# Kernel tuning notes

Hardware: AMD Instinct MI355X
Metric: run time of the kernel (lower is better)

Reference implementation:

```python
import jax, jax.numpy as jnp
import numpy as np

B, S, L, H, D, DF = 2, 1024, 2, 8, 512, 2048
DK = D // H  # head dim (dk == dv == 64)
EPS = 1e-5


def _ln(x, g, b):
    m = jnp.mean(x, axis=-1, keepdims=True)
    v = jnp.mean((x - m) ** 2, axis=-1, keepdims=True)
    return (x - m) / jnp.sqrt(v + EPS) * g + b


def setup_inputs() -> dict:
    key = jax.random.key(0)
    ks = jax.random.split(key, 8)
    sd = 1.0 / np.sqrt(D)
    sf = 1.0 / np.sqrt(DF)
    inp = {
        "src": jax.random.normal(ks[0], (B, S, D), jnp.float32),
        "Wq": jax.random.normal(ks[1], (L, D, D), jnp.float32) * sd,
        "bq": jnp.zeros((L, D), jnp.float32),
        "Wk": jax.random.normal(ks[2], (L, D, D), jnp.float32) * sd,
        "bk": jnp.zeros((L, D), jnp.float32),
        "Wv": jax.random.normal(ks[3], (L, D, D), jnp.float32) * sd,
        "bv": jnp.zeros((L, D), jnp.float32),
        "Wo": jax.random.normal(ks[4], (L, D, D), jnp.float32) * sd,
        "bo": jnp.zeros((L, D), jnp.float32),
        "W1": jax.random.normal(ks[5], (L, D, DF), jnp.float32) * sd,
        "b1": jnp.zeros((L, DF), jnp.float32),
        "W2": jax.random.normal(ks[6], (L, DF, D), jnp.float32) * sf,
        "b2": jnp.zeros((L, D), jnp.float32),
        "g1": jnp.ones((L, D), jnp.float32),
        "be1": jnp.zeros((L, D), jnp.float32),
        "g2": jnp.ones((L, D), jnp.float32),
        "be2": jnp.zeros((L, D), jnp.float32),
        "gf": jnp.ones((D,), jnp.float32),
        "bef": jnp.zeros((D,), jnp.float32),
    }
    return inp


def _heads(x):
    # [B,S,D] -> [B,H,S,DK]
    return x.reshape(B, S, H, DK).transpose(0, 2, 1, 3)


def _causal_linear_attention(q, k, v):
    # Faithful to torch: cumsum of per-step KV outer products, then query contraction.
    kv = jnp.einsum("bhsk,bhsv->bhskv", k, v)      # [B,H,S,DK,DK]
    cum = jnp.cumsum(kv, axis=2)                     # prefix sums over sequence
    return jnp.einsum("bhsk,bhskv->bhsv", q, cum)   # [B,H,S,DK]


def reference(src, Wq, bq, Wk, bk, Wv, bv, Wo, bo, W1, b1, W2, b2,
              g1, be1, g2, be2, gf, bef):
    x = src
    for i in range(L):
        q = _heads(x @ Wq[i] + bq[i])
        k = _heads(x @ Wk[i] + bk[i])
        v = _heads(x @ Wv[i] + bv[i])
        att = _causal_linear_attention(q, k, v)
        att = att.transpose(0, 2, 1, 3).reshape(B, S, D)
        att = att @ Wo[i] + bo[i]
        x = _ln(x + att, g1[i], be1[i])              # post-norm (normalize_before=False)
        ff = jax.nn.relu(x @ W1[i] + b1[i]) @ W2[i] + b2[i]
        x = _ln(x + ff, g2[i], be2[i])
    return _ln(x, gf, bef)                            # final encoder LayerNorm
```

## Files before the change

kernel.cpp:

```cpp
#include <hip/hip_runtime.h>
#include <hip/hip_bf16.h>

#define DEV static __device__ __forceinline__

typedef __attribute__((ext_vector_type(8))) short short8;
typedef __attribute__((ext_vector_type(4))) float f32x4;

DEV unsigned short f2b(float f){
  unsigned int u = __float_as_uint(f);
  return (unsigned short)((u + 0x7FFFu + ((u >> 16) & 1u)) >> 16);
}
DEV float b2f(unsigned short h){ return __uint_as_float(((unsigned int)h) << 16); }
DEV float load_in(const void* p, size_t i, int isbf){
  return isbf ? b2f(((const unsigned short*)p)[i]) : ((const float*)p)[i];
}
DEV void load_lds16(const unsigned short* g, unsigned short* l){
  __builtin_amdgcn_global_load_lds(
      (const __attribute__((address_space(1))) void*)g,
      (__attribute__((address_space(3))) void*)l, 16, 0, 0);
}

DEV int detect_isbf_block(const void* src){
  __shared__ int cnt[4];
  int tid = threadIdx.x;
  float v = b2f(((const unsigned short*)src)[2 * tid]);
  float av = fabsf(v);
  bool sane = ((av < 64.0f) && (av > 9.5e-7f)) || (v == 0.0f);
  unsigned long long m = __ballot(sane);
  if ((tid & 63) == 0) cnt[tid >> 6] = __popcll(m);
  __syncthreads();
  int tot = cnt[0] + cnt[1] + cnt[2] + cnt[3];
  __syncthreads();
  return tot > 128;
}

struct WDesc { const void* src; long src_off; unsigned short* dst; int K; int N; int tstart; };
struct SDesc { const void* src; int src_off; int dstart; };
struct IngestParams {
  WDesc w[12];
  SDesc s[22];
  float* sdst; int stotal;
  const void* src;
  float* xf; unsigned short* xb;
};

__global__ __launch_bounds__(256) void ingest_all(IngestParams P){
  __shared__ float tile[32][33];
  int b = blockIdx.x, tid = threadIdx.x;
  int isbf = detect_isbf_block(P.src);
  if (b < 6144){
    int t = 0;
    #pragma unroll
    for (int i = 1; i < 12; ++i) if (b >= P.w[i].tstart) t = i;
    WDesc d = P.w[t];
    int r = b - d.tstart;
    int tiles_x = d.N >> 5;
    int tx = r % tiles_x, ty = r / tiles_x;
    int lx = tid & 31, ly = tid >> 5;
    #pragma unroll
    for (int i = 0; i < 4; ++i){
      int row = ty*32 + ly + i*8;
      int col = tx*32 + lx;
      tile[ly + i*8][lx] = load_in(d.src, (size_t)d.src_off + (size_t)row*d.N + col, isbf);
    }
    __syncthreads();
    #pragma unroll
    for (int i = 0; i < 4; ++i){
      int orow = tx*32 + ly + i*8;
      int ocol = ty*32 + lx;
      d.dst[(size_t)orow*d.K + ocol] = f2b(tile[lx][ly + i*8]);
    }
    return;
  }
  int mb = b - 6144;
  if (mb < 4096){
    int i = mb*256 + tid;
    float v = load_in(P.src, (size_t)i, isbf);
    P.xf[i] = v; P.xb[i] = f2b(v);
  } else {
    int i = (mb - 4096)*256 + tid;
    if (i < P.stotal){
      int t = 0;
      #pragma unroll
      for (int j = 1; j < 22; ++j) if (i >= P.s[j].dstart) t = j;
      P.sdst[i] = load_in(P.s[t].src, (size_t)P.s[t].src_off + (i - P.s[t].dstart), isbf);
    }
  }
}

struct GemmArgs {
  const unsigned short* A;
  const unsigned short* Bt;
  const float* bias;
  float* Cf;
  unsigned short* Cb;
  int K;
  int lda, ldb, ldc;
  int cshift, cmask;
  size_t cstride;
  size_t cfz;
  int relu;
};

template<int BN>
__global__ __launch_bounds__(256) void gemm_bt(GemmArgs g){
  constexpr int NI = (BN == 128) ? 4 : 2;
  constexpr int NJ = 4;
  constexpr int BPASS = BN / 32;
  __shared__ __align__(16) unsigned short sA[2][128*64];
  __shared__ __align__(16) unsigned short sB[2][BN*64];
  int tid = threadIdx.x;
  int koff = blockIdx.z * g.K;
  int K = g.K, lda = g.lda, ldb = g.ldb;
  size_t bm = (size_t)blockIdx.y * 128, bn = (size_t)blockIdx.x * BN;
  int lane = tid & 63, wv = tid >> 6, quad = lane >> 4, l16 = lane & 15;
  int wm = (BN == 128) ? (wv >> 1) * 64 : wv * 32;
  int wn = (BN == 128) ? (wv & 1) * 64 : 0;
  f32x4 acc[NI][NJ];
  #pragma unroll
  for (int i=0;i<NI;++i)
    #pragma unroll
    for (int j=0;j<NJ;++j) acc[i][j] = (f32x4){0.f,0.f,0.f,0.f};
  int srow = tid >> 3;
  int schunk = (tid & 7) ^ (srow & 7);
  const unsigned short* Ap = g.A  + (bm + srow)*lda + koff + schunk*8;
  const unsigned short* Bp = g.Bt + (bn + srow)*ldb + koff + schunk*8;

  #define STAGE(buf, ko)                                                      \
    do {                                                                      \
      _Pragma("unroll")                                                       \
      for (int p = 0; p < 4; ++p)                                             \
        load_lds16(Ap + (size_t)(p*32)*lda + (ko), &sA[buf][p*2048 + tid*8]); \
      _Pragma("unroll")                                                       \
      for (int p = 0; p < BPASS; ++p)                                         \
        load_lds16(Bp + (size_t)(p*32)*ldb + (ko), &sB[buf][p*2048 + tid*8]); \
    } while (0)

  STAGE(0, 0);
  asm volatile("s_waitcnt vmcnt(0)" ::: "memory");
  __builtin_amdgcn_s_barrier();

  int nt = K >> 6;
  int cur = 0;
  for (int t = 0; t < nt; ++t){
    if (t + 1 < nt){
      STAGE(cur ^ 1, (t + 1) * 64);
      __builtin_amdgcn_sched_barrier(0);
    }
    #pragma unroll
    for (int kk = 0; kk < 2; ++kk){
      short8 af[NI], bfv[NJ];
      #pragma unroll
      for (int i=0;i<NI;++i){
        int row = wm + i*16 + l16;
        int ch  = (kk*4 + quad) ^ (row & 7);
        af[i] = *(const short8*)&sA[cur][row*64 + ch*8];
      }
      #pragma unroll
      for (int j=0;j<NJ;++j){
        int row = wn + j*16 + l16;
        int ch  = (kk*4 + quad) ^ (row & 7);
        bfv[j] = *(const short8*)&sB[cur][row*64 + ch*8];
      }
      #pragma unroll
      for (int i=0;i<NI;++i)
        #pragma unroll
        for (int j=0;j<NJ;++j)
          acc[i][j] = __builtin_amdgcn_mfma_f32_16x16x32_bf16(af[i], bfv[j], acc[i][j], 0,0,0);
    }
    if (t + 1 < nt){
      asm volatile("s_waitcnt vmcnt(0)" ::: "memory");
      __builtin_amdgcn_s_barrier();
    }
    cur ^= 1;
  }
  #undef STAGE

  float* Cf = g.Cf ? g.Cf + (size_t)blockIdx.z * g.cfz : nullptr;
  unsigned short* Cb = g.Cb;
  #pragma unroll
  for (int j=0;j<NJ;++j){
    int col = (int)bn + wn + j*16 + l16;
    float bv = g.bias ? g.bias[col] : 0.f;
    size_t cbase = ((size_t)(col >> g.cshift))*g.cstride + (col & g.cmask);
    #pragma unroll
    for (int i=0;i<NI;++i){
      #pragma unroll
      for (int r=0;r<4;++r){
        int row = (int)bm + wm + i*16 + quad*4 + r;
        float v = acc[i][j][r] + bv;
        if (g.relu) v = fmaxf(v, 0.f);
        size_t idx = cbase + (size_t)row*g.ldc;
        if (Cf) Cf[idx] = v;
        if (Cb) Cb[idx] = f2b(v);
      }
    }
  }
}

#define ATT_S 1024
#define ATT_D 512

__global__ __launch_bounds__(256) void attn_state_kernel(
    const unsigned short* k, const unsigned short* v, float* states)
{
  __shared__ __align__(16) unsigned short sVt[64*72];
  __shared__ __align__(16) unsigned short sKt[64*72];
  int tid = threadIdx.x;
  int c = blockIdx.x, bh = blockIdx.y;
  int b = bh >> 3, h = bh & 7;
  const size_t base = ((size_t)b*ATT_S + (size_t)c*64)*ATT_D + h*64;
  int lane = tid & 63, wv = tid >> 6, quad = lane >> 4, l16 = lane & 15;

  int t = lane, vc = wv*8;
  const unsigned short* vp = v + base + (size_t)t*ATT_D;
  const unsigned short* kp = k + base + (size_t)t*ATT_D;
  float4 v0 = *(const float4*)(vp + vc);
  float4 v1 = *(const float4*)(vp + vc + 32);
  float4 k0 = *(const float4*)(kp + vc);
  float4 k1 = *(const float4*)(kp + vc + 32);
  {
    const unsigned short* pv0 = (const unsigned short*)&v0;
    const unsigned short* pv1 = (const unsigned short*)&v1;
    const unsigned short* pk0 = (const unsigned short*)&k0;
    const unsigned short* pk1 = (const unsigned short*)&k1;
    #pragma unroll
    for (int e = 0; e < 8; ++e){
      sVt[(vc+e)*72 + t]    = pv0[e];
      sVt[(vc+32+e)*72 + t] = pv1[e];
      sKt[(vc+e)*72 + t]    = pk0[e];
      sKt[(vc+32+e)*72 + t] = pk1[e];
    }
  }
  __syncthreads();

  f32x4 acc[4];
  #pragma unroll
  for (int j=0;j<4;++j) acc[j] = (f32x4){0.f,0.f,0.f,0.f};
  #pragma unroll
  for (int kk=0;kk<2;++kk){
    short8 a = *(const short8*)&sVt[(wv*16 + l16)*72 + kk*32 + quad*8];
    #pragma unroll
    for (int j=0;j<4;++j){
      short8 bb = *(const short8*)&sKt[(j*16 + l16)*72 + kk*32 + quad*8];
      acc[j] = __builtin_amdgcn_mfma_f32_16x16x32_bf16(a, bb, acc[j], 0,0,0);
    }
  }
  float* st = states + ((size_t)bh*16 + c)*4096;
  #pragma unroll
  for (int j=0;j<4;++j)
    #pragma unroll
    for (int rr=0;rr<4;++rr)
      st[(wv*16 + quad*4 + rr)*64 + j*16 + l16] = acc[j][rr];
}

__global__ __launch_bounds__(256) void attn_out_kernel(
    const unsigned short* q, const unsigned short* k, const unsigned short* v,
    const float* states, unsigned short* att)
{
  __shared__ __align__(16) unsigned short sQ [64*72];
  __shared__ __align__(16) unsigned short sK [64*72];
  __shared__ __align__(16) unsigned short sVt[64*72];
  __shared__ __align__(16) float sKV[64*68];
  int tid = threadIdx.x;
  int c = blockIdx.x, bh = blockIdx.y;
  int b = bh >> 3, h = bh & 7;
  const size_t base = ((size_t)b*ATT_S + (size_t)c*64)*ATT_D + h*64;
  int lane = tid & 63, wv = tid >> 6, quad = lane >> 4, l16 = lane & 15;

  float4 racc[4];
  #pragma unroll
  for (int u=0;u<4;++u) racc[u] = (float4){0.f,0.f,0.f,0.f};
  const float* sbase = states + (size_t)bh*16*4096;
  for (int cc = 0; cc < c; ++cc){
    const float4* sp = (const float4*)(sbase + (size_t)cc*4096);
    #pragma unroll
    for (int u=0;u<4;++u){
      float4 t4 = sp[tid + u*256];
      racc[u].x += t4.x; racc[u].y += t4.y; racc[u].z += t4.z; racc[u].w += t4.w;
    }
  }
  #pragma unroll
  for (int u=0;u<4;++u){
    int e = (tid + u*256)*4;
    int row = e >> 6, col = e & 63;
    *(float4*)&sKV[row*68 + col] = racc[u];
  }

  int r = tid >> 2, c8 = (tid & 3)*8;
  const unsigned short* qp = q + base + (size_t)r*ATT_D;
  const unsigned short* kp = k + base + (size_t)r*ATT_D;
  float4 q0 = *(const float4*)(qp + c8);
  float4 q1 = *(const float4*)(qp + c8 + 32);
  float4 k0 = *(const float4*)(kp + c8);
  float4 k1 = *(const float4*)(kp + c8 + 32);
  int t = lane, vc = wv*8;
  const unsigned short* vp = v + base + (size_t)t*ATT_D;
  float4 v0 = *(const float4*)(vp + vc);
  float4 v1 = *(const float4*)(vp + vc + 32);
  *(float4*)&sQ[r*72 + c8]      = q0;
  *(float4*)&sQ[r*72 + c8 + 32] = q1;
  *(float4*)&sK[r*72 + c8]      = k0;
  *(float4*)&sK[r*72 + c8 + 32] = k1;
  {
    const unsigned short* pv0 = (const unsigned short*)&v0;
    const unsigned short* pv1 = (const unsigned short*)&v1;
    #pragma unroll
    for (int e=0;e<8;++e){
      sVt[(vc+e)*72 + t]    = pv0[e];
      sVt[(vc+32+e)*72 + t] = pv1[e];
    }
  }
  __syncthreads();

  f32x4 accS[4];
  #pragma unroll
  for (int j=0;j<4;++j) accS[j] = (f32x4){0.f,0.f,0.f,0.f};
  #pragma unroll
  for (int kk=0;kk<2;++kk){
    short8 a = *(const short8*)&sQ[(wv*16 + l16)*72 + kk*32 + quad*8];
    #pragma unroll
    for (int j=0;j<4;++j){
      short8 bb = *(const short8*)&sK[(j*16 + l16)*72 + kk*32 + quad*8];
      accS[j] = __builtin_amdgcn_mfma_f32_16x16x32_bf16(a, bb, accS[j], 0,0,0);
    }
  }
  __syncthreads();

  #pragma unroll
  for (int j=0;j<4;++j)
    #pragma unroll
    for (int rr=0;rr<4;++rr){
      int i  = wv*16 + quad*4 + rr;
      int cj = j*16 + l16;
      sK[i*72 + cj] = f2b((i >= cj) ? accS[j][rr] : 0.f);
    }

  f32x4 accO[4];
  #pragma unroll
  for (int j=0;j<4;++j) accO[j] = (f32x4){0.f,0.f,0.f,0.f};
  #pragma unroll
  for (int kk=0;kk<2;++kk){
    short8 a = *(const short8*)&sQ[(wv*16 + l16)*72 + kk*32 + quad*8];
    #pragma unroll
    for (int j=0;j<4;++j){
      const float* pf = &sKV[(j*16 + l16)*68 + kk*32 + quad*8];
      short8 bb;
      #pragma unroll
      for (int e=0;e<8;++e) ((unsigned short*)&bb)[e] = f2b(pf[e]);
      accO[j] = __builtin_amdgcn_mfma_f32_16x16x32_bf16(a, bb, accO[j], 0,0,0);
    }
  }
  __syncthreads();

  #pragma unroll
  for (int kk=0;kk<2;++kk){
    short8 a = *(const short8*)&sK[(wv*16 + l16)*72 + kk*32 + quad*8];
    #pragma unroll
    for (int j=0;j<4;++j){
      short8 bb = *(const short8*)&sVt[(j*16 + l16)*72 + kk*32 + quad*8];
      accO[j] = __builtin_amdgcn_mfma_f32_16x16x32_bf16(a, bb, accO[j], 0,0,0);
    }
  }
  #pragma unroll
  for (int j=0;j<4;++j)
    #pragma unroll
    for (int rr=0;rr<4;++rr){
      int i  = wv*16 + quad*4 + rr;
      int cj = j*16 + l16;
      att[base + (size_t)i*ATT_D + cj] = f2b(accO[j][rr]);
    }
}

__global__ __launch_bounds__(256) void add_ln_kernel(
    const float* x, const float* p, int np, const float* bias,
    const float* g, const float* bta, const float* g2, const float* b2,
    float* outf, unsigned short* outb, void* outd, const void* dsrc, int rows)
{
  int isbf = 0;
  if (dsrc) isbf = detect_isbf_block(dsrc);
  int row = blockIdx.x*4 + (threadIdx.x >> 6);
  int lane = threadIdx.x & 63;
  if (row >= rows) return;
  const float* xr = x + (size_t)row*512;
  float a[8];
  *(float4*)&a[0] = *(const float4*)(xr + lane*4);
  *(float4*)&a[4] = *(const float4*)(xr + 256 + lane*4);
  for (int s = 0; s < np; ++s){
    const float* pr = p + (size_t)s*1048576 + (size_t)row*512;
    float yb[8];
    *(float4*)&yb[0] = *(const float4*)(pr + lane*4);
    *(float4*)&yb[4] = *(const float4*)(pr + 256 + lane*4);
    #pragma unroll
    for (int e=0;e<8;++e) a[e] += yb[e];
  }
  if (bias){
    float bb2[8];
    *(float4*)&bb2[0] = *(const float4*)(bias + lane*4);
    *(float4*)&bb2[4] = *(const float4*)(bias + 256 + lane*4);
    #pragma unroll
    for (int e=0;e<8;++e) a[e] += bb2[e];
  }
  float s = 0.f, qq = 0.f;
  #pragma unroll
  for (int e=0;e<8;++e){ s += a[e]; qq += a[e]*a[e]; }
  #pragma unroll
  for (int off=32; off>0; off>>=1){
    s  += __shfl_xor(s,  off, 64);
    qq += __shfl_xor(qq, off, 64);
  }
  float mean = s * (1.f/512.f);
  float var  = qq * (1.f/512.f) - mean*mean;
  float rstd = rsqrtf(var + 1e-5f);
  float gg[8], bb[8];
  *(float4*)&gg[0] = *(const float4*)(g + lane*4);
  *(float4*)&gg[4] = *(const float4*)(g + 256 + lane*4);
  *(float4*)&bb[0] = *(const float4*)(bta + lane*4);
  *(float4*)&bb[4] = *(const float4*)(bta + 256 + lane*4);
  #pragma unroll
  for (int e=0;e<8;++e) a[e] = (a[e]-mean)*rstd*gg[e] + bb[e];
  if (g2){
    float s2 = 0.f, q2 = 0.f;
    #pragma unroll
    for (int e=0;e<8;++e){ s2 += a[e]; q2 += a[e]*a[e]; }
    #pragma unroll
    for (int off=32; off>0; off>>=1){
      s2 += __shfl_xor(s2, off, 64);
      q2 += __shfl_xor(q2, off, 64);
    }
    float m2 = s2 * (1.f/512.f);
    float v2 = q2 * (1.f/512.f) - m2*m2;
    float r2 = rsqrtf(v2 + 1e-5f);
    float gg2[8], bb22[8];
    *(float4*)&gg2[0]  = *(const float4*)(g2 + lane*4);
    *(float4*)&gg2[4]  = *(const float4*)(g2 + 256 + lane*4);
    *(float4*)&bb22[0] = *(const float4*)(b2 + lane*4);
    *(float4*)&bb22[4] = *(const float4*)(b2 + 256 + lane*4);
    #pragma unroll
    for (int e=0;e<8;++e) a[e] = (a[e]-m2)*r2*gg2[e] + bb22[e];
  }
  if (outf){
    float* orow = outf + (size_t)row*512;
    *(float4*)(orow + lane*4)       = *(float4*)&a[0];
    *(float4*)(orow + 256 + lane*4) = *(float4*)&a[4];
  }
  if (outb){
    unsigned short* orow = outb + (size_t)row*512;
    #pragma unroll
    for (int e=0;e<4;++e){ orow[lane*4+e] = f2b(a[e]); orow[256+lane*4+e] = f2b(a[4+e]); }
  }
  if (outd){
    if (isbf){
      unsigned short* od = (unsigned short*)outd + (size_t)row*512;
      #pragma unroll
      for (int e=0;e<4;++e){ od[lane*4+e] = f2b(a[e]); od[256+lane*4+e] = f2b(a[4+e]); }
    } else {
      float* od = (float*)outd + (size_t)row*512;
      *(float4*)(od + lane*4)       = *(float4*)&a[0];
      *(float4*)(od + 256 + lane*4) = *(float4*)&a[4];
    }
  }
}

extern "C" void kernel_launch(void* const* d_in, const int* in_sizes, int n_in,
                              void* d_out, int out_size, void* d_ws, size_t ws_size,
                              hipStream_t stream)
{
  (void)in_sizes; (void)n_in; (void)out_size; (void)ws_size;
  const void* src = d_in[0];
  const void* Wq = d_in[1];  const void* bq = d_in[2];
  const void* Wk = d_in[3];  const void* bk = d_in[4];
  const void* Wv = d_in[5];  const void* bv = d_in[6];
  const void* Wo = d_in[7];  const void* bo = d_in[8];
  const void* W1 = d_in[9];  const void* b1 = d_in[10];
  const void* W2 = d_in[11]; const void* b2 = d_in[12];
  const void* g1 = d_in[13]; const void* be1 = d_in[14];
  const void* g2 = d_in[15]; const void* be2 = d_in[16];
  const void* gf = d_in[17]; const void* bef = d_in[18];

  char* W = (char*)d_ws;
  float* smalls          = (float*)(W + 256);
  unsigned short* wt     = (unsigned short*)(W + 65536);
  float* x_f             = (float*)(W + 12648448);
  unsigned short* x_b    = (unsigned short*)(W + 16842752);
  unsigned short* q_b    = (unsigned short*)(W + 18939904);
  unsigned short* att_b  = (unsigned short*)(W + 25231360);
  float* pp              = (float*)(W + 27328512);
  unsigned short* h1_b   = (unsigned short*)(W + 44105728);
  float* states          = (float*)(W + 44105728);
  unsigned short* k_b = q_b + 1048576;
  unsigned short* v_b = q_b + 2097152;

  IngestParams ip;
  {
    const void* wsrc[6] = {Wq, Wk, Wv, Wo, W1, W2};
    int wK[6] = {512,512,512,512,512,2048};
    int wN[6] = {512,512,512,512,2048,512};
    long wsz[6] = {262144,262144,262144,262144,1048576,1048576};
    int tstart = 0; size_t dsto = 0;
    for (int l=0;l<2;++l)
      for (int ti=0;ti<6;++ti){
        int idx = l*6+ti;
        ip.w[idx].src = wsrc[ti];
        ip.w[idx].src_off = (long)l * wsz[ti];
        ip.w[idx].dst = wt + dsto;
        ip.w[idx].K = wK[ti]; ip.w[idx].N = wN[ti];
        ip.w[idx].tstart = tstart;
        tstart += (wK[ti]/32)*(wN[ti]/32);
        dsto += (size_t)wsz[ti];
      }
    const void* ss[10] = {bq,bk,bv,bo,b1,b2,g1,be1,g2,be2};
    int slen[10] = {512,512,512,512,2048,512,512,512,512,512};
    int dcur = 0, di = 0;
    for (int l=0;l<2;++l)
      for (int ti=0;ti<10;++ti){
        ip.s[di].src = ss[ti];
        ip.s[di].src_off = l * slen[ti];
        ip.s[di].dstart = dcur;
        dcur += slen[ti]; ++di;
      }
    ip.s[20].src = gf;  ip.s[20].src_off = 0; ip.s[20].dstart = dcur; dcur += 512;
    ip.s[21].src = bef; ip.s[21].src_off = 0; ip.s[21].dstart = dcur; dcur += 512;
    ip.sdst = smalls; ip.stotal = dcur;
    ip.src = src; ip.xf = x_f; ip.xb = x_b;
    ingest_all<<<dim3(10296), 256, 0, stream>>>(ip);
  }

  for (int l = 0; l < 2; ++l){
    unsigned short* WqkvT = wt + (size_t)l*3145728;
    unsigned short* WoT   = WqkvT + 786432;
    unsigned short* W1T   = WqkvT + 1048576;
    unsigned short* W2T   = WqkvT + 2097152;
    float* base  = smalls + l*6656;
    float* p_bqkv= base;
    float* p_bo  = base + 1536;
    float* p_b1  = base + 2048;
    float* p_b2  = base + 4096;
    float* p_g1  = base + 4608;
    float* p_be1 = base + 5120;
    float* p_g2  = base + 5632;
    float* p_be2 = base + 6144;

    GemmArgs qkv = {};
    qkv.A = x_b; qkv.Bt = WqkvT; qkv.bias = p_bqkv;
    qkv.Cf = nullptr; qkv.Cb = q_b;
    qkv.K = 512; qkv.lda = 512; qkv.ldb = 512; qkv.ldc = 512;
    qkv.cshift = 9; qkv.cmask = 511; qkv.cstride = 1048576; qkv.cfz = 0; qkv.relu = 0;
    gemm_bt<64><<<dim3(24,16,1), 256, 0, stream>>>(qkv);

    attn_state_kernel<<<dim3(16,16), 256, 0, stream>>>(k_b, v_b, states);
    attn_out_kernel<<<dim3(16,16), 256, 0, stream>>>(q_b, k_b, v_b, states, att_b);

    GemmArgs go = {};
    go.A = att_b; go.Bt = WoT; go.bias = nullptr;
    go.Cf = pp; go.Cb = nullptr;
    go.K = 256; go.lda = 512; go.ldb = 512; go.ldc = 512;
    go.cshift = 30; go.cmask = 0x3fffffff; go.cstride = 0; go.cfz = 1048576; go.relu = 0;
    gemm_bt<64><<<dim3(8,16,2), 256, 0, stream>>>(go);

    add_ln_kernel<<<dim3(512), 256, 0, stream>>>(x_f, pp, 2, p_bo, p_g1, p_be1,
                                                 nullptr, nullptr,
                                                 x_f, x_b, nullptr, nullptr, 2048);

    GemmArgs f1 = {};
    f1.A = x_b; f1.Bt = W1T; f1.bias = p_b1;
    f1.Cf = nullptr; f1.Cb = h1_b;
    f1.K = 512; f1.lda = 512; f1.ldb = 512; f1.ldc = 2048;
    f1.cshift = 30; f1.cmask = 0x3fffffff; f1.cstride = 0; f1.cfz = 0; f1.relu = 1;
    gemm_bt<64><<<dim3(32,16,1), 256, 0, stream>>>(f1);

    GemmArgs f2 = {};
    f2.A = h1_b; f2.Bt = W2T; f2.bias = nullptr;
    f2.Cf = pp; f2.Cb = nullptr;
    f2.K = 1024; f2.lda = 2048; f2.ldb = 2048; f2.ldc = 512;
    f2.cshift = 30; f2.cmask = 0x3fffffff; f2.cstride = 0; f2.cfz = 1048576; f2.relu = 0;
    gemm_bt<64><<<dim3(8,16,2), 256, 0, stream>>>(f2);

    if (l == 0){
      add_ln_kernel<<<dim3(512), 256, 0, stream>>>(x_f, pp, 2, p_b2, p_g2, p_be2,
                                                   nullptr, nullptr,
                                                   x_f, x_b, nullptr, nullptr, 2048);
    } else {
      add_ln_kernel<<<dim3(512), 256, 0, stream>>>(x_f, pp, 2, p_b2, p_g2, p_be2,
                                                   smalls + 13312, smalls + 13824,
                                                   nullptr, nullptr, d_out, src, 2048);
    }
  }
}
```

Measured before the change: 257.2 us.

## Split FFN2 GEMM over four K-slices and read residual from source

The second FFN GEMM is split into four K-slices of 512 instead of two of 1024. This launches twice as many blocks, and the following add+LayerNorm now sums four partial outputs. Separately, the ingest kernel no longer writes an fp32 copy of the input; the first layer's attention add+LayerNorm reads the residual directly from the source buffer. That source may be bf16 or fp32, detected at runtime. The changes trade extra partial-sum traffic for better GPU occupancy and remove one write pass.

```diff
diff --git a/kernel.cpp b/kernel.cpp
--- a/kernel.cpp
+++ b/kernel.cpp
@@ -41,7 +41,7 @@
   SDesc s[22];
   float* sdst; int stotal;
   const void* src;
-  float* xf; unsigned short* xb;
+  unsigned short* xb;
 };
 
 __global__ __launch_bounds__(256) void ingest_all(IngestParams P){
@@ -75,8 +75,7 @@
   int mb = b - 6144;
   if (mb < 4096){
     int i = mb*256 + tid;
-    float v = load_in(P.src, (size_t)i, isbf);
-    P.xf[i] = v; P.xb[i] = f2b(v);
+    P.xb[i] = f2b(load_in(P.src, (size_t)i, isbf));
   } else {
     int i = (mb - 4096)*256 + tid;
     if (i < P.stotal){
@@ -373,7 +372,7 @@
 }
 
 __global__ __launch_bounds__(256) void add_ln_kernel(
-    const float* x, const float* p, int np, const float* bias,
+    const float* x, const void* xalt, const float* p, int np, const float* bias,
     const float* g, const float* bta, const float* g2, const float* b2,
     float* outf, unsigned short* outb, void* outd, const void* dsrc, int rows)
 {
@@ -382,10 +381,26 @@
   int row = blockIdx.x*4 + (threadIdx.x >> 6);
   int lane = threadIdx.x & 63;
   if (row >= rows) return;
-  const float* xr = x + (size_t)row*512;
   float a[8];
-  *(float4*)&a[0] = *(const float4*)(xr + lane*4);
-  *(float4*)&a[4] = *(const float4*)(xr + 256 + lane*4);
+  if (xalt){
+    if (isbf){
+      const unsigned short* xr = (const unsigned short*)xalt + (size_t)row*512;
+      short8 u0 = *(const short8*)(xr + lane*4*2);
+      const unsigned short* p0 = xr + lane*4;
+      const unsigned short* p1 = xr + 256 + lane*4;
+      (void)u0;
+      #pragma unroll
+      for (int e=0;e<4;++e){ a[e] = b2f(p0[e]); a[4+e] = b2f(p1[e]); }
+    } else {
+      const float* xr = (const float*)xalt + (size_t)row*512;
+      *(float4*)&a[0] = *(const float4*)(xr + lane*4);
+      *(float4*)&a[4] = *(const float4*)(xr + 256 + lane*4);
+    }
+  } else {
+    const float* xr = x + (size_t)row*512;
+    *(float4*)&a[0] = *(const float4*)(xr + lane*4);
+    *(float4*)&a[4] = *(const float4*)(xr + 256 + lane*4);
+  }
   for (int s = 0; s < np; ++s){
     const float* pr = p + (size_t)s*1048576 + (size_t)row*512;
     float yb[8];
@@ -522,7 +537,7 @@
     ip.s[20].src = gf;  ip.s[20].src_off = 0; ip.s[20].dstart = dcur; dcur += 512;
     ip.s[21].src = bef; ip.s[21].src_off = 0; ip.s[21].dstart = dcur; dcur += 512;
     ip.sdst = smalls; ip.stotal = dcur;
-    ip.src = src; ip.xf = x_f; ip.xb = x_b;
+    ip.src = src; ip.xb = x_b;
     ingest_all<<<dim3(10296), 256, 0, stream>>>(ip);
   }
 
@@ -558,9 +573,14 @@
     go.cshift = 30; go.cmask = 0x3fffffff; go.cstride = 0; go.cfz = 1048576; go.relu = 0;
     gemm_bt<64><<<dim3(8,16,2), 256, 0, stream>>>(go);
 
-    add_ln_kernel<<<dim3(512), 256, 0, stream>>>(x_f, pp, 2, p_bo, p_g1, p_be1,
-                                                 nullptr, nullptr,
-                                                 x_f, x_b, nullptr, nullptr, 2048);
+    if (l == 0)
+      add_ln_kernel<<<dim3(512), 256, 0, stream>>>(nullptr, src, pp, 2, p_bo,
+                                                   p_g1, p_be1, nullptr, nullptr,
+                                                   x_f, x_b, nullptr, src, 2048);
+    else
+      add_ln_kernel<<<dim3(512), 256, 0, stream>>>(x_f, nullptr, pp, 2, p_bo,
+                                                   p_g1, p_be1, nullptr, nullptr,
+                                                   x_f, x_b, nullptr, nullptr, 2048);
 
     GemmArgs f1 = {};
     f1.A = x_b; f1.Bt = W1T; f1.bias = p_b1;
@@ -572,16 +592,17 @@
     GemmArgs f2 = {};
     f2.A = h1_b; f2.Bt = W2T; f2.bias = nullptr;
     f2.Cf = pp; f2.Cb = nullptr;
-    f2.K = 1024; f2.lda = 2048; f2.ldb = 2048; f2.ldc = 512;
+    f2.K = 512; f2.lda = 2048; f2.ldb = 2048; f2.ldc = 512;
     f2.cshift = 30; f2.cmask = 0x3fffffff; f2.cstride = 0; f2.cfz = 1048576; f2.relu = 0;
-    gemm_bt<64><<<dim3(8,16,2), 256, 0, stream>>>(f2);
+    gemm_bt<64><<<dim3(8,16,4), 256, 0, stream>>>(f2);
 
     if (l == 0){
-      add_ln_kernel<<<dim3(512), 256, 0, stream>>>(x_f, pp, 2, p_b2, p_g2, p_be2,
-                                                   nullptr, nullptr,
+      add_ln_kernel<<<dim3(512), 256, 0, stream>>>(x_f, nullptr, pp, 4, p_b2,
+                                                   p_g2, p_be2, nullptr, nullptr,
                                                    x_f, x_b, nullptr, nullptr, 2048);
     } else {
-      add_ln_kernel<<<dim3(512), 256, 0, stream>>>(x_f, pp, 2, p_b2, p_g2, p_be2,
+      add_ln_kernel<<<dim3(512), 256, 0, stream>>>(x_f, nullptr, pp, 4, p_b2,
+                                                   p_g2, p_be2,
                                                    smalls + 13312, smalls + 13824,
                                                    nullptr, nullptr, d_out, src, 2048);
     }
```

Result: no change. 253.4 us (-1.5%).
